# Performance work log

Hardware: AMD Instinct MI355X
Metric: run time of the kernel (lower is better)

## Reference

```python
import jax, jax.numpy as jnp
import numpy as np

B, H, C = 1, 4, 32
D = H * C          # 128
S, L = 128, 256
EPS = 1e-5


def _axial_layer_norm(x, gamma, beta):
    # normalize over channel axis (axis=1) of [B, D, S, L]
    mu = jnp.mean(x, axis=1, keepdims=True)
    var = jnp.var(x, axis=1, keepdims=True)
    xn = (x - mu) * jax.lax.rsqrt(var + EPS)
    return xn * gamma[None, :, None, None] + beta[None, :, None, None]


def setup_inputs() -> dict:
    key = jax.random.key(0)
    ks = jax.random.split(key, 5)
    x = jax.random.normal(ks[0], (B, D, S, L), dtype=jnp.float32)
    w_row = jax.random.normal(ks[1], (3 * D, D), dtype=jnp.float32) * 0.02
    b_row = jax.random.normal(ks[2], (3 * D,), dtype=jnp.float32) * 0.02
    w_col = jax.random.normal(ks[3], (3 * D, D), dtype=jnp.float32) * 0.02
    b_col = jax.random.normal(ks[4], (3 * D,), dtype=jnp.float32) * 0.02
    return {
        "x": x,
        "w_row": w_row, "b_row": b_row,
        "w_col": w_col, "b_col": b_col,
        "gamma1": jnp.ones((D,), jnp.float32), "beta1": jnp.zeros((D,), jnp.float32),
        "gamma2": jnp.ones((D,), jnp.float32), "beta2": jnp.zeros((D,), jnp.float32),
    }


def _qkv(x, w, b):
    # 1x1 conv == channel matmul: [3D, D] x [B, D, S, L] -> [B, 3D, S, L]
    qkv = jnp.einsum('od,bdsl->bosl', w, x) + b[None, :, None, None]
    q, k, v = jnp.split(qkv, 3, axis=1)
    rs = lambda t: t.reshape(t.shape[0], H, C, S, L)
    return rs(q), rs(k), rs(v)


def reference(x, w_row, b_row, w_col, b_col, gamma1, beta1, gamma2, beta2):
    # --- row attention (attend along L within each row s) ---
    q, k, v = _qkv(x, w_row, b_row)
    row_attn = jnp.einsum('bhcsi,bhcsj->bhsij', q, k)   # [B,H,S,L,L], no 1/sqrt(d) scaling (as in source)
    row_attn = jax.nn.softmax(row_attn, axis=-1)
    row_out = jnp.einsum('bhsij,bhdsj->bhdsi', row_attn, v).reshape(x.shape[0], D, S, L)
    out = _axial_layer_norm(x + row_out, gamma1, beta1)

    # --- column attention (attend along S within each column l) ---
    q, k, v = _qkv(out, w_col, b_col)
    col_attn = jnp.einsum('bhcil,bhcjl->bhijl', q, k)   # [B,H,S,S,L]
    col_attn = jax.nn.softmax(col_attn, axis=-2)
    col_out = jnp.einsum('bhijl,bhdjl->bhdil', col_attn, v).reshape(x.shape[0], D, S, L)
    out = _axial_layer_norm(out + col_out, gamma2, beta2)
    return out
```

## Files before the change

### kernel.cpp

```cpp
#include <hip/hip_runtime.h>
#include <hip/hip_bf16.h>

#define SL     32768
#define EPS_LN 1e-5f

typedef unsigned short u16;
typedef __attribute__((ext_vector_type(8))) short bf16x8;
typedef __attribute__((ext_vector_type(4))) float f32x4;

#define MFMA16(a, b, c) __builtin_amdgcn_mfma_f32_16x16x32_bf16((a), (b), (c), 0, 0, 0)

__device__ inline u16 f2bf(float f) {
    __hip_bfloat16 h = __float2bfloat16(f);
    return *reinterpret_cast<u16*>(&h);
}
__device__ inline float bf2f(u16 u) {
    unsigned v = ((unsigned)u) << 16;
    float f;
    __builtin_memcpy(&f, &v, 4);
    return f;
}
__device__ inline uint4 pack8(float4 a, float4 b) {
    union { uint4 v; u16 u[8]; } U;
    U.u[0] = f2bf(a.x); U.u[1] = f2bf(a.y); U.u[2] = f2bf(a.z); U.u[3] = f2bf(a.w);
    U.u[4] = f2bf(b.x); U.u[5] = f2bf(b.y); U.u[6] = f2bf(b.z); U.u[7] = f2bf(b.w);
    return U.v;
}

__global__ __launch_bounds__(256) void wcast_kernel(const float* __restrict__ wr,
                                                    const float* __restrict__ wc,
                                                    u16* __restrict__ wrb,
                                                    u16* __restrict__ wcb) {
    const int i = blockIdx.x * 256 + threadIdx.x;
    const int NW = 384 * 128 / 8;
    const float* src = (i < NW) ? wr : wc;
    u16* dst = (i < NW) ? wrb : wcb;
    const int j = (i < NW) ? i : i - NW;
    float4 a = ((const float4*)src)[j * 2];
    float4 b = ((const float4*)src)[j * 2 + 1];
    ((uint4*)dst)[j] = pack8(a, b);
}

template<int LAYOUT>
__global__ __launch_bounds__(512) void qkv_mfma(const void* __restrict__ inv,
                                                const u16* __restrict__ wb,
                                                const float* __restrict__ bq,
                                                u16* __restrict__ qT,
                                                u16* __restrict__ kT,
                                                u16* __restrict__ vb) {
    __shared__ u16 xT[64][136];
    __shared__ float bs[384];
    const int n0 = blockIdx.x * 64;
    const int t = threadIdx.x;
    const int lane = t & 63, wv = t >> 6, lo = lane & 15, hi = lane >> 4;

    if (t < 384) bs[t] = bq[t];

    if constexpr (LAYOUT == 0) {
        #pragma unroll
        for (int itr = 0; itr < 2; ++itr) {
            const int u = t + itr * 512;
            const int d = u & 127, noct = u >> 7;
            const float* src = (const float*)inv + (size_t)d * SL + n0 + noct * 8;
            float4 f0 = *(const float4*)src;
            float4 f1 = *(const float4*)(src + 4);
            xT[noct * 8 + 0][d] = f2bf(f0.x);
            xT[noct * 8 + 1][d] = f2bf(f0.y);
            xT[noct * 8 + 2][d] = f2bf(f0.z);
            xT[noct * 8 + 3][d] = f2bf(f0.w);
            xT[noct * 8 + 4][d] = f2bf(f1.x);
            xT[noct * 8 + 5][d] = f2bf(f1.y);
            xT[noct * 8 + 6][d] = f2bf(f1.z);
            xT[noct * 8 + 7][d] = f2bf(f1.w);
        }
    } else {
        #pragma unroll
        for (int itr = 0; itr < 2; ++itr) {
            const int u = t + itr * 512;
            const int n = u >> 4, seg = u & 15;
            *(uint4*)&xT[n][seg * 8] =
                *(const uint4*)((const u16*)inv + (size_t)(n0 + n) * 128 + seg * 8);
        }
    }
    __syncthreads();

    bf16x8 af[3][4];
    #pragma unroll
    for (int om = 0; om < 3; ++om)
        #pragma unroll
        for (int ks = 0; ks < 4; ++ks)
            af[om][ks] = *(const bf16x8*)(wb + (size_t)(wv * 48 + om * 16 + lo) * 128
                                             + hi * 8 + ks * 32);

    #pragma unroll
    for (int nt = 0; nt < 4; ++nt) {
        const int n = n0 + nt * 16 + lo;
        bf16x8 bfr[4];
        #pragma unroll
        for (int ks = 0; ks < 4; ++ks)
            bfr[ks] = *(const bf16x8*)&xT[nt * 16 + lo][hi * 8 + ks * 32];
        #pragma unroll
        for (int om = 0; om < 3; ++om) {
            const int obase = wv * 48 + om * 16;
            f32x4 acc = {0.f, 0.f, 0.f, 0.f};
            #pragma unroll
            for (int ks = 0; ks < 4; ++ks)
                acc = MFMA16(af[om][ks], bfr[ks], acc);
            if (obase < 256) {
                u16* tbuf = (obase < 128) ? qT : kT;
                const int ob = obase & 127;
                const int h = ob >> 5;
                const int cb = (ob & 31) + hi * 4;
                ushort4 o4;
                o4.x = f2bf(acc[0] + bs[obase + hi * 4 + 0]);
                o4.y = f2bf(acc[1] + bs[obase + hi * 4 + 1]);
                o4.z = f2bf(acc[2] + bs[obase + hi * 4 + 2]);
                o4.w = f2bf(acc[3] + bs[obase + hi * 4 + 3]);
                *(ushort4*)(tbuf + (size_t)h * SL * 32 + (size_t)n * 32 + cb) = o4;
            } else {
                const int orow = obase - 256 + hi * 4;
                #pragma unroll
                for (int r = 0; r < 4; ++r)
                    vb[(size_t)(orow + r) * SL + n] = f2bf(acc[r] + bs[obase + hi * 4 + r]);
            }
        }
    }
}

template<int KLEN, int NTHR>
__global__ __launch_bounds__(NTHR) void attn_kernel(const u16* __restrict__ qT,
                                                    const u16* __restrict__ kT,
                                                    const u16* __restrict__ vb,
                                                    u16* __restrict__ ao) {
    constexpr int NJT = KLEN / 16;
    constexpr int NW = NTHR / 64;
    constexpr int NOUT = SL / KLEN;
    __shared__ u16 PT[NW][2][16][36];

    const int bid = blockIdx.x;
    const int outer = bid % NOUT;
    const int h = bid / NOUT;
    const int base = outer * KLEN;
    const int t = threadIdx.x;
    const int lane = t & 63, wv = t >> 6, lo = lane & 15, hi = lane >> 4;
    const int i0w = wv * 32;

    const u16* qh = qT + (size_t)h * SL * 32;
    const u16* kh = kT + (size_t)h * SL * 32;
    const u16* vh = vb + (size_t)h * 32 * SL;

    bf16x8 qf0 = *(const bf16x8*)(qh + (size_t)(base + i0w + lo) * 32 + hi * 8);
    bf16x8 qf1 = *(const bf16x8*)(qh + (size_t)(base + i0w + 16 + lo) * 32 + hi * 8);

    f32x4 o00 = {0.f, 0.f, 0.f, 0.f}, o01 = {0.f, 0.f, 0.f, 0.f};
    f32x4 o10 = {0.f, 0.f, 0.f, 0.f}, o11 = {0.f, 0.f, 0.f, 0.f};
    float ls0[4] = {0.f, 0.f, 0.f, 0.f};
    float ls1[4] = {0.f, 0.f, 0.f, 0.f};

    #pragma unroll
    for (int jt = 0; jt < NJT; ++jt) {
        bf16x8 kf = *(const bf16x8*)(kh + (size_t)(base + jt * 16 + lo) * 32 + hi * 8);
        f32x4 z = {0.f, 0.f, 0.f, 0.f};
        f32x4 s0 = MFMA16(qf0, kf, z);
        f32x4 s1 = MFMA16(qf1, kf, z);
        #pragma unroll
        for (int r = 0; r < 4; ++r) {
            float p0 = __expf(s0[r]);
            ls0[r] += p0;
            PT[wv][0][hi * 4 + r][(jt & 1) * 16 + lo] = f2bf(p0);
            float p1 = __expf(s1[r]);
            ls1[r] += p1;
            PT[wv][1][hi * 4 + r][(jt & 1) * 16 + lo] = f2bf(p1);
        }
        if (jt & 1) {
            const int jb = (jt - 1) * 16;
            bf16x8 pf0 = *(const bf16x8*)&PT[wv][0][lo][hi * 8];
            bf16x8 pf1 = *(const bf16x8*)&PT[wv][1][lo][hi * 8];
            bf16x8 v0 = *(const bf16x8*)(vh + (size_t)lo * SL + base + jb + hi * 8);
            bf16x8 v1 = *(const bf16x8*)(vh + (size_t)(16 + lo) * SL + base + jb + hi * 8);
            o00 = MFMA16(pf0, v0, o00);
            o01 = MFMA16(pf0, v1, o01);
            o10 = MFMA16(pf1, v0, o10);
            o11 = MFMA16(pf1, v1, o11);
        }
    }
    #pragma unroll
    for (int r = 0; r < 4; ++r) {
        float v0 = ls0[r];
        v0 += __shfl_xor(v0, 1);
        v0 += __shfl_xor(v0, 2);
        v0 += __shfl_xor(v0, 4);
        v0 += __shfl_xor(v0, 8);
        ls0[r] = 1.f / v0;
        float v1 = ls1[r];
        v1 += __shfl_xor(v1, 1);
        v1 += __shfl_xor(v1, 2);
        v1 += __shfl_xor(v1, 4);
        v1 += __shfl_xor(v1, 8);
        ls1[r] = 1.f / v1;
    }
    {
        ushort4 o4;
        o4.x = f2bf(o00[0] * ls0[0]);
        o4.y = f2bf(o00[1] * ls0[1]);
        o4.z = f2bf(o00[2] * ls0[2]);
        o4.w = f2bf(o00[3] * ls0[3]);
        *(ushort4*)(ao + (size_t)(h * 32 + lo) * SL + base + i0w + hi * 4) = o4;
        o4.x = f2bf(o01[0] * ls0[0]);
        o4.y = f2bf(o01[1] * ls0[1]);
        o4.z = f2bf(o01[2] * ls0[2]);
        o4.w = f2bf(o01[3] * ls0[3]);
        *(ushort4*)(ao + (size_t)(h * 32 + 16 + lo) * SL + base + i0w + hi * 4) = o4;
        o4.x = f2bf(o10[0] * ls1[0]);
        o4.y = f2bf(o10[1] * ls1[1]);
        o4.z = f2bf(o10[2] * ls1[2]);
        o4.w = f2bf(o10[3] * ls1[3]);
        *(ushort4*)(ao + (size_t)(h * 32 + lo) * SL + base + i0w + 16 + hi * 4) = o4;
        o4.x = f2bf(o11[0] * ls1[0]);
        o4.y = f2bf(o11[1] * ls1[1]);
        o4.z = f2bf(o11[2] * ls1[2]);
        o4.w = f2bf(o11[3] * ls1[3]);
        *(ushort4*)(ao + (size_t)(h * 32 + 16 + lo) * SL + base + i0w + 16 + hi * 4) = o4;
    }
}

__global__ __launch_bounds__(256) void ln_mid(const float* __restrict__ in0,
                                              const u16* __restrict__ in1,
                                              const float* __restrict__ g,
                                              const float* __restrict__ be,
                                              u16* __restrict__ outp) {
    __shared__ float val[128][69];
    __shared__ float redS[4][72];
    __shared__ float redQ[4][72];
    __shared__ float stat[64][2];
    __shared__ float gs[128], bes[128];
    const int bid = blockIdx.x;
    const int r0 = (bid / 16) * 4;
    const int c0 = (bid % 16) * 16;
    const int t = threadIdx.x;
    const int pos = t & 63, q = t >> 6;
    const size_t gp = (size_t)(r0 + (pos >> 4)) * 256 + c0 + (pos & 15);

    if (t < 128) { gs[t] = g[t]; bes[t] = be[t]; }
    float s = 0.f, ss = 0.f;
    #pragma unroll 4
    for (int dd = 0; dd < 32; ++dd) {
        const int d = q * 32 + dd;
        float v = in0[(size_t)d * SL + gp] + bf2f(in1[(size_t)d * SL + gp]);
        val[d][pos] = v;
        s += v; ss += v * v;
    }
    redS[q][pos] = s;
    redQ[q][pos] = ss;
    __syncthreads();
    if (t < 64) {
        const float S  = redS[0][t] + redS[1][t] + redS[2][t] + redS[3][t];
        const float SS = redQ[0][t] + redQ[1][t] + redQ[2][t] + redQ[3][t];
        const float mean = S * (1.f / 128.f);
        const float var  = SS * (1.f / 128.f) - mean * mean;
        stat[t][0] = mean;
        stat[t][1] = rsqrtf(var + EPS_LN);
    }
    __syncthreads();

    {
        const int pr = pos >> 4, pc = pos & 15;
        const size_t pp = (size_t)(c0 + pc) * 128 + r0 + pr;
        const float mean = stat[pos][0], rstd = stat[pos][1];
        union { uint4 v[4]; u16 u[32]; } O;
        #pragma unroll
        for (int dd = 0; dd < 32; ++dd) {
            const int d = q * 32 + dd;
            O.u[dd] = f2bf((val[d][pos] - mean) * rstd * gs[d] + bes[d]);
        }
        uint4* dst = (uint4*)(outp + pp * 128 + q * 32);
        #pragma unroll
        for (int k = 0; k < 4; ++k) dst[k] = O.v[k];
    }
}

__global__ __launch_bounds__(256) void ln_out(const u16* __restrict__ in0,
                                              const u16* __restrict__ in1,
                                              const float* __restrict__ g,
                                              const float* __restrict__ be,
                                              float* __restrict__ outp) {
    __shared__ float val[128][69];
    __shared__ float redS[4][72];
    __shared__ float redQ[4][72];
    __shared__ float stat[64][2];
    const int bid = blockIdx.x;
    const int r0 = (bid / 8) * 4;
    const int c0 = (bid % 8) * 16;
    const int t = threadIdx.x;
    const int pos = t & 63, q = t >> 6;
    const size_t gp = (size_t)(r0 + (pos >> 4)) * 128 + c0 + (pos & 15);

    float s = 0.f, ss = 0.f;
    {
        union { uint4 v[4]; u16 u[32]; } A;
        const uint4* src = (const uint4*)(in0 + gp * 128 + q * 32);
        #pragma unroll
        for (int k = 0; k < 4; ++k) A.v[k] = src[k];
        #pragma unroll 4
        for (int dd = 0; dd < 32; ++dd) {
            const int d = q * 32 + dd;
            float v = bf2f(A.u[dd]) + bf2f(in1[(size_t)d * SL + gp]);
            val[d][pos] = v;
            s += v; ss += v * v;
        }
    }
    redS[q][pos] = s;
    redQ[q][pos] = ss;
    __syncthreads();
    if (t < 64) {
        const float S  = redS[0][t] + redS[1][t] + redS[2][t] + redS[3][t];
        const float SS = redQ[0][t] + redQ[1][t] + redQ[2][t] + redQ[3][t];
        const float mean = S * (1.f / 128.f);
        const float var  = SS * (1.f / 128.f) - mean * mean;
        stat[t][0] = mean;
        stat[t][1] = rsqrtf(var + EPS_LN);
    }
    __syncthreads();

    {
        const int d = t >> 1;
        const int ch = (t & 1) * 8;
        const float gd = g[d], bd = be[d];
        #pragma unroll
        for (int cc = 0; cc < 8; ++cc) {
            const int c = ch + cc;
            float ov[4];
            #pragma unroll
            for (int r = 0; r < 4; ++r) {
                const int p = r * 16 + c;
                ov[r] = (val[d][p] - stat[p][0]) * stat[p][1] * gd + bd;
            }
            float* dst = outp + (size_t)d * SL + (c0 + c) * 256 + r0;
            *(float4*)dst = make_float4(ov[0], ov[1], ov[2], ov[3]);
        }
    }
}

extern "C" void kernel_launch(void* const* d_in, const int* in_sizes, int n_in,
                              void* d_out, int out_size, void* d_ws, size_t ws_size,
                              hipStream_t stream) {
    const float* x     = (const float*)d_in[0];
    const float* w_row = (const float*)d_in[1];
    const float* b_row = (const float*)d_in[2];
    const float* w_col = (const float*)d_in[3];
    const float* b_col = (const float*)d_in[4];
    const float* g1    = (const float*)d_in[5];
    const float* be1   = (const float*)d_in[6];
    const float* g2    = (const float*)d_in[7];
    const float* be2   = (const float*)d_in[8];
    float* out = (float*)d_out;

    char* base = (char*)d_ws;
    u16* qTb = (u16*)base;                        base += (size_t)128 * SL * 2;
    u16* kTb = (u16*)base;                        base += (size_t)128 * SL * 2;
    u16* vbb = (u16*)base;                        base += (size_t)128 * SL * 2;
    u16* ao16 = (u16*)base;                       base += (size_t)128 * SL * 2;
    u16* o1b  = (u16*)base;                       base += (size_t)128 * SL * 2;
    u16* wrb  = (u16*)base;                       base += (size_t)384 * 128 * 2;
    u16* wcb  = (u16*)base;

    wcast_kernel<<<48, 256, 0, stream>>>(w_row, w_col, wrb, wcb);
    qkv_mfma<0><<<512, 512, 0, stream>>>(x, wrb, b_row, qTb, kTb, vbb);
    attn_kernel<256, 512><<<512, 512, 0, stream>>>(qTb, kTb, vbb, ao16);
    ln_mid<<<512, 256, 0, stream>>>(x, ao16, g1, be1, o1b);
    qkv_mfma<1><<<512, 512, 0, stream>>>(o1b, wcb, b_col, qTb, kTb, vbb);
    attn_kernel<128, 256><<<1024, 256, 0, stream>>>(qTb, kTb, vbb, ao16);
    ln_out<<<512, 256, 0, stream>>>(o1b, ao16, g2, be2, out);
}
```

Measured before the change: 98.70 us.

## Fuse column-attention QKV projection and attention into one kernel

Measured after the change: 91.56 us, median of 3. -7.2%, faster.

```diff
diff --git a/kernel.cpp b/kernel.cpp
--- a/kernel.cpp
+++ b/kernel.cpp
@@ -41,8 +41,7 @@
     ((uint4*)dst)[j] = pack8(a, b);
 }
 
-template<int LAYOUT>
-__global__ __launch_bounds__(512) void qkv_mfma(const void* __restrict__ inv,
+__global__ __launch_bounds__(512) void qkv_mfma(const float* __restrict__ in,
                                                 const u16* __restrict__ wb,
                                                 const float* __restrict__ bq,
                                                 u16* __restrict__ qT,
@@ -56,31 +55,21 @@
 
     if (t < 384) bs[t] = bq[t];
 
-    if constexpr (LAYOUT == 0) {
-        #pragma unroll
-        for (int itr = 0; itr < 2; ++itr) {
-            const int u = t + itr * 512;
-            const int d = u & 127, noct = u >> 7;
-            const float* src = (const float*)inv + (size_t)d * SL + n0 + noct * 8;
-            float4 f0 = *(const float4*)src;
-            float4 f1 = *(const float4*)(src + 4);
-            xT[noct * 8 + 0][d] = f2bf(f0.x);
-            xT[noct * 8 + 1][d] = f2bf(f0.y);
-            xT[noct * 8 + 2][d] = f2bf(f0.z);
-            xT[noct * 8 + 3][d] = f2bf(f0.w);
-            xT[noct * 8 + 4][d] = f2bf(f1.x);
-            xT[noct * 8 + 5][d] = f2bf(f1.y);
-            xT[noct * 8 + 6][d] = f2bf(f1.z);
-            xT[noct * 8 + 7][d] = f2bf(f1.w);
-        }
-    } else {
-        #pragma unroll
-        for (int itr = 0; itr < 2; ++itr) {
-            const int u = t + itr * 512;
-            const int n = u >> 4, seg = u & 15;
-            *(uint4*)&xT[n][seg * 8] =
-                *(const uint4*)((const u16*)inv + (size_t)(n0 + n) * 128 + seg * 8);
-        }
+    #pragma unroll
+    for (int itr = 0; itr < 2; ++itr) {
+        const int u = t + itr * 512;
+        const int d = u & 127, noct = u >> 7;
+        const float* src = in + (size_t)d * SL + n0 + noct * 8;
+        float4 f0 = *(const float4*)src;
+        float4 f1 = *(const float4*)(src + 4);
+        xT[noct * 8 + 0][d] = f2bf(f0.x);
+        xT[noct * 8 + 1][d] = f2bf(f0.y);
+        xT[noct * 8 + 2][d] = f2bf(f0.z);
+        xT[noct * 8 + 3][d] = f2bf(f0.w);
+        xT[noct * 8 + 4][d] = f2bf(f1.x);
+        xT[noct * 8 + 5][d] = f2bf(f1.y);
+        xT[noct * 8 + 6][d] = f2bf(f1.z);
+        xT[noct * 8 + 7][d] = f2bf(f1.w);
     }
     __syncthreads();
 
@@ -224,6 +213,148 @@
     }
 }
 
+__global__ __launch_bounds__(512) void qkv_attn2(const u16* __restrict__ in,
+                                                 const u16* __restrict__ wb,
+                                                 const float* __restrict__ bq,
+                                                 u16* __restrict__ ao) {
+    __shared__ u16 xS[128][136];
+    __shared__ u16 qkS[2][4][128][36];
+    __shared__ u16 vS[4][32][136];
+    __shared__ u16 PT[8][2][16][36];
+    __shared__ float bs[384];
+
+    const int l = blockIdx.x;
+    const size_t p0 = (size_t)l * 128;
+    const int t = threadIdx.x;
+    const int lane = t & 63, wv = t >> 6, lo = lane & 15, hi = lane >> 4;
+
+    if (t < 384) bs[t] = bq[t];
+    #pragma unroll
+    for (int itr = 0; itr < 4; ++itr) {
+        const int u = t + itr * 512;
+        const int n = u >> 4, seg = u & 15;
+        *(uint4*)&xS[n][seg * 8] = *(const uint4*)(in + (p0 + n) * 128 + seg * 8);
+    }
+    __syncthreads();
+
+    bf16x8 af[3][4];
+    #pragma unroll
+    for (int om = 0; om < 3; ++om)
+        #pragma unroll
+        for (int ks = 0; ks < 4; ++ks)
+            af[om][ks] = *(const bf16x8*)(wb + (size_t)(wv * 48 + om * 16 + lo) * 128
+                                             + hi * 8 + ks * 32);
+    #pragma unroll
+    for (int nt = 0; nt < 8; ++nt) {
+        const int n = nt * 16 + lo;
+        bf16x8 bfr[4];
+        #pragma unroll
+        for (int ks = 0; ks < 4; ++ks)
+            bfr[ks] = *(const bf16x8*)&xS[n][hi * 8 + ks * 32];
+        #pragma unroll
+        for (int om = 0; om < 3; ++om) {
+            const int obase = wv * 48 + om * 16;
+            f32x4 acc = {0.f, 0.f, 0.f, 0.f};
+            #pragma unroll
+            for (int ks = 0; ks < 4; ++ks)
+                acc = MFMA16(af[om][ks], bfr[ks], acc);
+            if (obase < 256) {
+                const int qk = obase >> 7;
+                const int ob = obase & 127;
+                const int h = ob >> 5;
+                const int cb = (ob & 31) + hi * 4;
+                ushort4 o4;
+                o4.x = f2bf(acc[0] + bs[obase + hi * 4 + 0]);
+                o4.y = f2bf(acc[1] + bs[obase + hi * 4 + 1]);
+                o4.z = f2bf(acc[2] + bs[obase + hi * 4 + 2]);
+                o4.w = f2bf(acc[3] + bs[obase + hi * 4 + 3]);
+                *(ushort4*)&qkS[qk][h][n][cb] = o4;
+            } else {
+                const int vr = obase - 256 + hi * 4;
+                #pragma unroll
+                for (int r = 0; r < 4; ++r) {
+                    const int o = vr + r;
+                    vS[o >> 5][o & 31][n] = f2bf(acc[r] + bs[obase + hi * 4 + r]);
+                }
+            }
+        }
+    }
+    __syncthreads();
+
+    const int h = wv >> 1;
+    u16 (*oS)[136] = xS;
+
+    #pragma unroll
+    for (int g = 0; g < 2; ++g) {
+        const int ib = (wv & 1) * 64 + g * 32;
+        bf16x8 qf0 = *(const bf16x8*)&qkS[0][h][ib + lo][hi * 8];
+        bf16x8 qf1 = *(const bf16x8*)&qkS[0][h][ib + 16 + lo][hi * 8];
+
+        f32x4 o00 = {0.f, 0.f, 0.f, 0.f}, o01 = {0.f, 0.f, 0.f, 0.f};
+        f32x4 o10 = {0.f, 0.f, 0.f, 0.f}, o11 = {0.f, 0.f, 0.f, 0.f};
+        float ls0[4] = {0.f, 0.f, 0.f, 0.f};
+        float ls1[4] = {0.f, 0.f, 0.f, 0.f};
+
+        #pragma unroll
+        for (int jt = 0; jt < 8; ++jt) {
+            bf16x8 kf = *(const bf16x8*)&qkS[1][h][jt * 16 + lo][hi * 8];
+            f32x4 z = {0.f, 0.f, 0.f, 0.f};
+            f32x4 s0 = MFMA16(qf0, kf, z);
+            f32x4 s1 = MFMA16(qf1, kf, z);
+            #pragma unroll
+            for (int r = 0; r < 4; ++r) {
+                float pv0 = __expf(s0[r]);
+                ls0[r] += pv0;
+                PT[wv][0][hi * 4 + r][(jt & 1) * 16 + lo] = f2bf(pv0);
+                float pv1 = __expf(s1[r]);
+                ls1[r] += pv1;
+                PT[wv][1][hi * 4 + r][(jt & 1) * 16 + lo] = f2bf(pv1);
+            }
+            if (jt & 1) {
+                const int jb = (jt - 1) * 16;
+                bf16x8 pf0 = *(const bf16x8*)&PT[wv][0][lo][hi * 8];
+                bf16x8 pf1 = *(const bf16x8*)&PT[wv][1][lo][hi * 8];
+                bf16x8 v0 = *(const bf16x8*)&vS[h][lo][jb + hi * 8];
+                bf16x8 v1 = *(const bf16x8*)&vS[h][16 + lo][jb + hi * 8];
+                o00 = MFMA16(pf0, v0, o00);
+                o01 = MFMA16(pf0, v1, o01);
+                o10 = MFMA16(pf1, v0, o10);
+                o11 = MFMA16(pf1, v1, o11);
+            }
+        }
+        #pragma unroll
+        for (int r = 0; r < 4; ++r) {
+            float v0 = ls0[r];
+            v0 += __shfl_xor(v0, 1);
+            v0 += __shfl_xor(v0, 2);
+            v0 += __shfl_xor(v0, 4);
+            v0 += __shfl_xor(v0, 8);
+            ls0[r] = 1.f / v0;
+            float v1 = ls1[r];
+            v1 += __shfl_xor(v1, 1);
+            v1 += __shfl_xor(v1, 2);
+            v1 += __shfl_xor(v1, 4);
+            v1 += __shfl_xor(v1, 8);
+            ls1[r] = 1.f / v1;
+        }
+        #pragma unroll
+        for (int r = 0; r < 4; ++r) {
+            oS[h * 32 + lo][ib + hi * 4 + r]           = f2bf(o00[r] * ls0[r]);
+            oS[h * 32 + 16 + lo][ib + hi * 4 + r]      = f2bf(o01[r] * ls0[r]);
+            oS[h * 32 + lo][ib + 16 + hi * 4 + r]      = f2bf(o10[r] * ls1[r]);
+            oS[h * 32 + 16 + lo][ib + 16 + hi * 4 + r] = f2bf(o11[r] * ls1[r]);
+        }
+    }
+    __syncthreads();
+
+    #pragma unroll
+    for (int itr = 0; itr < 4; ++itr) {
+        const int u = t + itr * 512;
+        const int ch = u >> 4, seg = u & 15;
+        *(uint4*)(ao + (size_t)ch * SL + p0 + seg * 8) = *(const uint4*)&oS[ch][seg * 8];
+    }
+}
+
 __global__ __launch_bounds__(256) void ln_mid(const float* __restrict__ in0,
                                               const u16* __restrict__ in1,
                                               const float* __restrict__ g,
@@ -365,10 +496,9 @@
     u16* wcb  = (u16*)base;
 
     wcast_kernel<<<48, 256, 0, stream>>>(w_row, w_col, wrb, wcb);
-    qkv_mfma<0><<<512, 512, 0, stream>>>(x, wrb, b_row, qTb, kTb, vbb);
+    qkv_mfma<<<512, 512, 0, stream>>>(x, wrb, b_row, qTb, kTb, vbb);
     attn_kernel<256, 512><<<512, 512, 0, stream>>>(qTb, kTb, vbb, ao16);
     ln_mid<<<512, 256, 0, stream>>>(x, ao16, g1, be1, o1b);
-    qkv_mfma<1><<<512, 512, 0, stream>>>(o1b, wcb, b_col, qTb, kTb, vbb);
-    attn_kernel<128, 256><<<1024, 256, 0, stream>>>(qTb, kTb, vbb, ao16);
+    qkv_attn2<<<256, 512, 0, stream>>>(o1b, wcb, b_col, ao16);
     ln_out<<<512, 256, 0, stream>>>(o1b, ao16, g2, be2, out);
 }
```
